# Kernel optimization log

Measured on AMD Instinct MI355X. Metric: run time of the kernel, lower is better.

## Reference

```python
import jax, jax.numpy as jnp
import numpy as np

B, N, C, H, K = 16, 2048, 64, 128, 16
EPS = 1e-5  # torch BatchNorm1d default eps


def _bn(h, g, b, axes):
    # training-mode batch norm: biased variance over all non-channel axes
    m = h.mean(axes, keepdims=True)
    v = h.var(axes, keepdims=True)
    return (h - m) * jax.lax.rsqrt(v + EPS) * g + b


def _edge_conv(x, W1, b1, g1, be1, W2, b2, g2, be2):
    # x: [B, N, C]; dynamic kNN graph in feature space (per graph), includes self
    sq = jnp.sum(x * x, axis=-1)                                   # [B, N]
    d2 = sq[:, :, None] + sq[:, None, :] - 2.0 * jnp.einsum('bnc,bmc->bnm', x, x)
    idx = jax.lax.top_k(-d2, K)[1]                                 # [B, N, K]
    xj = jax.vmap(lambda xb, ib: xb[ib])(x, idx)                   # [B, N, K, C]
    xi = jnp.broadcast_to(x[:, :, None, :], xj.shape)
    h = jnp.concatenate([xi, xj - xi], axis=-1) @ W1 + b1          # [B, N, K, H]
    h = jax.nn.relu(_bn(h, g1, be1, (0, 1, 2)))
    h = h @ W2 + b2
    h = jax.nn.relu(_bn(h, g2, be2, (0, 1, 2)))
    return h.max(axis=2)                                           # max aggregation -> [B, N, H]


def setup_inputs() -> dict:
    key = jax.random.key(0)
    ks = jax.random.split(key, 8)
    inp = {
        'x': jax.random.normal(ks[0], (B * N, C), jnp.float32),
        'batch': jnp.repeat(jnp.arange(B, dtype=jnp.int32), N),
    }
    i = 1
    for pref in ('s', 't'):
        inp[f'{pref}_W1'] = jax.random.normal(ks[i], (2 * C, H), jnp.float32) * 0.05; i += 1
        inp[f'{pref}_b1'] = jnp.zeros((H,), jnp.float32)
        inp[f'{pref}_g1'] = jnp.ones((H,), jnp.float32)
        inp[f'{pref}_be1'] = jnp.zeros((H,), jnp.float32)
        inp[f'{pref}_W2'] = jax.random.normal(ks[i], (H, H), jnp.float32) * 0.05; i += 1
        inp[f'{pref}_b2'] = jnp.zeros((H,), jnp.float32)
        inp[f'{pref}_g2'] = jnp.ones((H,), jnp.float32)
        inp[f'{pref}_be2'] = jnp.zeros((H,), jnp.float32)
    inp['f_W'] = jax.random.normal(ks[i], (2 * H, H), jnp.float32) * 0.05
    inp['f_b'] = jnp.zeros((H,), jnp.float32)
    inp['f_g'] = jnp.ones((H,), jnp.float32)
    inp['f_be'] = jnp.zeros((H,), jnp.float32)
    return inp


def reference(x, batch,
              s_W1, s_b1, s_g1, s_be1, s_W2, s_b2, s_g2, s_be2,
              t_W1, t_b1, t_g1, t_be1, t_W2, t_b2, t_g2, t_be2,
              f_W, f_b, f_g, f_be):
    # batch is sorted with B equal-size graphs of N nodes -> reshape
    xb = x.reshape(B, N, C)
    xs = _edge_conv(xb, s_W1, s_b1, s_g1, s_be1, s_W2, s_b2, s_g2, s_be2)
    xt = _edge_conv(xb, t_W1, t_b1, t_g1, t_be1, t_W2, t_b2, t_g2, t_be2)
    comb = jnp.concatenate([xs, xt], axis=-1).reshape(B * N, 2 * H)
    h = comb @ f_W + f_b
    return jax.nn.relu(_bn(h, f_g, f_be, (0,)))
```

## Files before the change

kernel.cpp:

```cpp
#include <hip/hip_runtime.h>
#include <hip/hip_bf16.h>
#include <stdint.h>

#define NB 16
#define NN 2048
#define NC 64
#define NH 128
#define NK 16
#define NS (NB*NN)
#define NSK (NS*NK)
#define EPSV 1e-5f

typedef __attribute__((ext_vector_type(8))) short short8;
typedef __attribute__((ext_vector_type(8))) _Float16 half8;
typedef __attribute__((ext_vector_type(8))) unsigned short ushort8;
typedef __attribute__((ext_vector_type(4))) float f32x4;

__device__ __forceinline__ unsigned short f2bf(float x) {
  union { float f; unsigned u; } v; v.f = x;
  unsigned r = v.u + 0x7fffu + ((v.u >> 16) & 1u);
  return (unsigned short)(r >> 16);
}

__device__ __forceinline__ unsigned orderf(float f) {
  unsigned u = __float_as_uint(f);
  return u ^ ((unsigned)((int)u >> 31) | 0x80000000u);
}

__device__ __forceinline__ float unorderf(unsigned whi) {
  return (whi == 0xffffffffu) ? __builtin_inff()
       : __uint_as_float((whi & 0x80000000u) ? (whi ^ 0x80000000u) : ~whi);
}

__device__ __forceinline__ unsigned long long shfl_xor_u64(unsigned long long v, int m) {
  unsigned lo = (unsigned)(v & 0xffffffffull);
  unsigned hi = (unsigned)(v >> 32);
  lo = __shfl_xor(lo, m, 64);
  hi = __shfl_xor(hi, m, 64);
  return (((unsigned long long)hi) << 32) | lo;
}

__global__ void prep_x(const float* __restrict__ x, float* __restrict__ sq,
                       unsigned short* __restrict__ xh, unsigned short* __restrict__ xl) {
  int i = blockIdx.x * blockDim.x + threadIdx.x;
  if (i >= NS) return;
  const float4* x4 = (const float4*)(x + (size_t)i * NC);
  float s = 0.f;
#pragma unroll
  for (int k = 0; k < 8; k++) {
    float4 a = x4[2*k], b = x4[2*k+1];
    float f[8] = {a.x,a.y,a.z,a.w,b.x,b.y,b.z,b.w};
    ushort8 hv, lv;
#pragma unroll
    for (int j = 0; j < 8; j++) {
      float v = f[j];
      s += v*v;
      _Float16 h = (_Float16)v;
      float r = v - (float)h;
      _Float16 l = (_Float16)r;
      union { _Float16 ff; unsigned short u; } ch, cl;
      ch.ff = h; cl.ff = l;
      hv[j] = ch.u; lv[j] = cl.u;
    }
    *(ushort8*)(xh + (size_t)i*64 + k*8) = hv;
    *(ushort8*)(xl + (size_t)i*64 + k*8) = lv;
  }
  sq[i] = s;
}

__global__ __launch_bounds__(256) void knn5_kernel(const unsigned short* __restrict__ xh,
                                                   const unsigned short* __restrict__ xl,
                                                   const float* __restrict__ sq,
                                                   int* __restrict__ nbr) {
  __shared__ unsigned short rAh[64*64], rAl[64*64];
  __shared__ unsigned short cBh[64*64], cBl[64*64];
  __shared__ float sqc[64];
  __shared__ float d2s[256*17];
  int b = blockIdx.x >> 5;
  int rb = blockIdx.x & 31;
  int w = threadIdx.x >> 6, lane = threadIdx.x & 63;
  int n16 = lane & 15, q = lane >> 4;
  int rowbase = b*NN + rb*64;
  float* myd2 = &d2s[threadIdx.x * 17];

  {
    int r = threadIdx.x >> 2;
    int c0 = (threadIdx.x & 3) * 2;
#pragma unroll
    for (int cc = 0; cc < 2; cc++) {
      int c = c0 + cc;
      int pos = (c ^ (r & 7)) * 8;
      *(ushort8*)&rAh[r*64 + pos] = *(const ushort8*)(xh + (size_t)(rowbase + r)*64 + c*8);
      *(ushort8*)&rAl[r*64 + pos] = *(const ushort8*)(xl + (size_t)(rowbase + r)*64 + c*8);
    }
  }
  __syncthreads();
  half8 bh[2], bl[2];
  int m = w*16 + n16;
#pragma unroll
  for (int ks = 0; ks < 2; ks++) {
    int pos = ((ks*4 + q) ^ (m & 7)) * 8;
    bh[ks] = *(const half8*)&rAh[m*64 + pos];
    bl[ks] = *(const half8*)&rAl[m*64 + pos];
  }
  float sqr = sq[rowbase + m];

  unsigned long long keys[16];
#pragma unroll
  for (int i = 0; i < 16; i++) keys[i] = ~0ull;
  float wd2 = __builtin_inff();

  for (int ch = 0; ch < 32; ch++) {
    int colbase = b*NN + ch*64;
    __syncthreads();
    {
      int r = threadIdx.x >> 2;
      int c0 = (threadIdx.x & 3) * 2;
#pragma unroll
      for (int cc = 0; cc < 2; cc++) {
        int c = c0 + cc;
        int pos = (c ^ (r & 7)) * 8;
        *(ushort8*)&cBh[r*64 + pos] = *(const ushort8*)(xh + (size_t)(colbase + r)*64 + c*8);
        *(ushort8*)&cBl[r*64 + pos] = *(const ushort8*)(xl + (size_t)(colbase + r)*64 + c*8);
      }
      if (threadIdx.x < 64) sqc[threadIdx.x] = sq[colbase + threadIdx.x];
    }
    __syncthreads();
    f32x4 acc[4];
#pragma unroll
    for (int ci = 0; ci < 4; ci++) acc[ci] = (f32x4){0.f,0.f,0.f,0.f};
#pragma unroll
    for (int ks = 0; ks < 2; ks++) {
#pragma unroll
      for (int ci = 0; ci < 4; ci++) {
        int n = ci*16 + n16;
        int pos = ((ks*4 + q) ^ (n & 7)) * 8;
        half8 ah_ = *(const half8*)&cBh[n*64 + pos];
        half8 al_ = *(const half8*)&cBl[n*64 + pos];
        acc[ci] = __builtin_amdgcn_mfma_f32_16x16x32_f16(ah_, bh[ks], acc[ci], 0, 0, 0);
        acc[ci] = __builtin_amdgcn_mfma_f32_16x16x32_f16(al_, bh[ks], acc[ci], 0, 0, 0);
        acc[ci] = __builtin_amdgcn_mfma_f32_16x16x32_f16(ah_, bl[ks], acc[ci], 0, 0, 0);
      }
    }
    float d2v[16];
    unsigned mask = 0;
#pragma unroll
    for (int ci = 0; ci < 4; ci++)
#pragma unroll
      for (int r = 0; r < 4; r++) {
        int idx = ci*4 + r;
        float d2 = fmaf(-2.f, acc[ci][r], sqr + sqc[ci*16 + q*4 + r]);
        d2v[idx] = d2;
        mask |= (d2 <= wd2) ? (1u << idx) : 0u;
      }
    if (mask) {
#pragma unroll
      for (int i = 0; i < 16; i++) myd2[i] = d2v[i];
      while (mask) {
        int i = __builtin_ctz(mask);
        mask &= mask - 1;
        float dd = myd2[i];
        if (dd > wd2) continue;
        int col = colbase + (i >> 2)*16 + q*4 + (i & 3);
        unsigned long long key = ((unsigned long long)orderf(dd) << 32) | (unsigned)col;
#pragma unroll
        for (int j = 0; j < 16; j++) {
          bool cl = key < keys[j];
          unsigned long long lo = cl ? key : keys[j];
          key = cl ? keys[j] : key;
          keys[j] = lo;
        }
        wd2 = fminf(wd2, unorderf((unsigned)(keys[15] >> 32)));
      }
    }
    {
      unsigned whi = (unsigned)(keys[15] >> 32);
      unsigned o = __shfl_xor(whi, 16, 64); whi = (o < whi) ? o : whi;
      o = __shfl_xor(whi, 32, 64); whi = (o < whi) ? o : whi;
      wd2 = unorderf(whi);
    }
  }
  for (int j = 0; j < NK; j++) {
    unsigned long long mk = keys[0];
#pragma unroll
    for (int i = 1; i < 16; i++) mk = (keys[i] < mk) ? keys[i] : mk;
    unsigned long long o = shfl_xor_u64(mk, 16); mk = (o < mk) ? o : mk;
    o = shfl_xor_u64(mk, 32); mk = (o < mk) ? o : mk;
#pragma unroll
    for (int i = 0; i < 16; i++) if (keys[i] == mk) keys[i] = ~0ull;
    if (q == 0) nbr[(size_t)(rowbase + m)*NK + j] = (int)(mk & 0xffffffffu);
  }
}

__global__ void prep_weights(const float* __restrict__ sW1, const float* __restrict__ sW2,
                             const float* __restrict__ tW1, const float* __restrict__ tW2,
                             const float* __restrict__ fW,
                             unsigned short* __restrict__ sW1t, unsigned short* __restrict__ sW2t,
                             unsigned short* __restrict__ tW1t, unsigned short* __restrict__ tW2t,
                             unsigned short* __restrict__ fWt) {
  int i = blockIdx.x * blockDim.x + threadIdx.x;
  if (i < 4*16384) {
    int mi = i >> 14, e = i & 16383;
    int h = e >> 7, k = e & 127;
    const float* src = (mi==0) ? sW1 : (mi==1) ? sW2 : (mi==2) ? tW1 : tW2;
    unsigned short* dst = (mi==0) ? sW1t : (mi==1) ? sW2t : (mi==2) ? tW1t : tW2t;
    dst[h*128 + k] = f2bf(src[k*128 + h]);
  } else {
    int e = i - 4*16384;
    if (e < 128*256) {
      int h = e >> 8, k = e & 255;
      fWt[h*256 + k] = f2bf(fW[k*128 + h]);
    }
  }
}

__global__ __launch_bounds__(256) void pnode_kernel(
    const float* __restrict__ x,
    const unsigned short* __restrict__ sW1t, const unsigned short* __restrict__ tW1t,
    float* __restrict__ PS, float* __restrict__ PT) {
  __shared__ unsigned short xt_[64*64];
  int rowbase = blockIdx.x * 64;
  int lane = threadIdx.x & 63;
  int wave = threadIdx.x >> 6;
  int n16 = lane & 15, q = lane >> 4;
  int cb = wave * 32;
  {
    int r = threadIdx.x >> 2, part = threadIdx.x & 3;
    const float4* xp = (const float4*)(x + (size_t)(rowbase + r) * NC) + part*4;
#pragma unroll
    for (int cc = 0; cc < 2; cc++) {
      int c = part*2 + cc;
      float4 a = xp[cc*2], b = xp[cc*2+1];
      int pos = (c ^ (r & 7)) * 8;
      unsigned short* d = &xt_[r*64 + pos];
      d[0]=f2bf(a.x); d[1]=f2bf(a.y); d[2]=f2bf(a.z); d[3]=f2bf(a.w);
      d[4]=f2bf(b.x); d[5]=f2bf(b.y); d[6]=f2bf(b.z); d[7]=f2bf(b.w);
    }
  }
  __syncthreads();
  f32x4 aS[4][2], aT[4][2];
#pragma unroll
  for (int ri = 0; ri < 4; ri++)
#pragma unroll
    for (int ci = 0; ci < 2; ci++) {
      aS[ri][ci] = (f32x4){0.f,0.f,0.f,0.f};
      aT[ri][ci] = (f32x4){0.f,0.f,0.f,0.f};
    }
#pragma unroll
  for (int ks = 0; ks < 2; ks++) {
    short8 af[4];
#pragma unroll
    for (int ri = 0; ri < 4; ri++) {
      int m = ri*16 + n16;
      af[ri] = *(const short8*)&xt_[m*64 + (((ks*4+q) ^ (m & 7)))*8];
    }
#pragma unroll
    for (int ci = 0; ci < 2; ci++) {
      int col = cb + ci*16 + n16;
      short8 bS = *(const short8*)(sW1t + col*128 + (ks*4+q)*8);
      short8 bT = *(const short8*)(tW1t + col*128 + (ks*4+q)*8);
#pragma unroll
      for (int ri = 0; ri < 4; ri++) {
        aS[ri][ci] = __builtin_amdgcn_mfma_f32_16x16x32_bf16(af[ri], bS, aS[ri][ci], 0, 0, 0);
        aT[ri][ci] = __builtin_amdgcn_mfma_f32_16x16x32_bf16(af[ri], bT, aT[ri][ci], 0, 0, 0);
      }
    }
  }
#pragma unroll
  for (int ri = 0; ri < 4; ri++)
#pragma unroll
    for (int ci = 0; ci < 2; ci++) {
      int col = cb + ci*16 + n16;
#pragma unroll
      for (int r = 0; r < 4; r++) {
        int row = rowbase + ri*16 + q*4 + r;
        PS[(size_t)row*128 + col] = aS[ri][ci][r];
        PT[(size_t)row*128 + col] = aT[ri][ci][r];
      }
    }
}

__global__ __launch_bounds__(256, 2) void dstat_kernel(
    const float* __restrict__ x, const int* __restrict__ nbr,
    const unsigned short* __restrict__ sW1t, const unsigned short* __restrict__ tW1t,
    const float* __restrict__ PS, const float* __restrict__ PT,
    unsigned short* __restrict__ D,
    float* __restrict__ statS, float* __restrict__ statT) {
  __shared__ unsigned short dlds[64*64];
  int wave = threadIdx.x >> 6, lane = threadIdx.x & 63;
  int n16 = lane & 15, q = lane >> 4;
  int cb = wave * 32;
  int g = blockIdx.x & 15, sub = blockIdx.x >> 4;
  float psS[2]={0,0}, ps2S[2]={0,0}, psT[2]={0,0}, ps2T[2]={0,0};

  for (int it = 0; it < 4; it++) {
    int tile = g*512 + sub*4 + it;
    __syncthreads();
    {
      int r4 = threadIdx.x >> 2, part = threadIdx.x & 3;
      int s = tile*64 + r4;
      int node = s >> 4;
      int ng = nbr[s];
      const float4* xi = (const float4*)(x + (size_t)node * NC) + part*4;
      const float4* xj = (const float4*)(x + (size_t)ng  * NC) + part*4;
      unsigned short* dstg = D + (size_t)tile*4096 + (size_t)r4*64;
#pragma unroll
      for (int cc = 0; cc < 2; cc++) {
        int c = part*2 + cc;
        float4 a0 = xi[cc*2], a1 = xi[cc*2+1];
        float4 b0 = xj[cc*2], b1 = xj[cc*2+1];
        int pos = (c ^ (r4 & 7)) * 8;
        ushort8 dv;
        dv[0]=f2bf(b0.x-a0.x); dv[1]=f2bf(b0.y-a0.y); dv[2]=f2bf(b0.z-a0.z); dv[3]=f2bf(b0.w-a0.w);
        dv[4]=f2bf(b1.x-a1.x); dv[5]=f2bf(b1.y-a1.y); dv[6]=f2bf(b1.z-a1.z); dv[7]=f2bf(b1.w-a1.w);
        *(ushort8*)(dstg + pos) = dv;
        *(ushort8*)(dlds + r4*64 + pos) = dv;
      }
    }
    __syncthreads();
    int node0 = tile*4;
    float pS[4][2], pT[4][2];
#pragma unroll
    for (int ri = 0; ri < 4; ri++)
#pragma unroll
      for (int ci = 0; ci < 2; ci++) {
        int col = cb + ci*16 + n16;
        pS[ri][ci] = PS[(size_t)(node0+ri)*128 + col];
        pT[ri][ci] = PT[(size_t)(node0+ri)*128 + col];
      }
    f32x4 aS[4][2], aT[4][2];
#pragma unroll
    for (int ri = 0; ri < 4; ri++)
#pragma unroll
      for (int ci = 0; ci < 2; ci++) {
        aS[ri][ci] = (f32x4){0.f,0.f,0.f,0.f};
        aT[ri][ci] = (f32x4){0.f,0.f,0.f,0.f};
      }
#pragma unroll
    for (int ks = 0; ks < 2; ks++) {
      short8 af[4];
#pragma unroll
      for (int ri = 0; ri < 4; ri++) {
        int m = ri*16 + n16;
        af[ri] = *(const short8*)&dlds[m*64 + ((ks*4+q) ^ (m & 7))*8];
      }
#pragma unroll
      for (int ci = 0; ci < 2; ci++) {
        int col = cb + ci*16 + n16;
        short8 bS = *(const short8*)(sW1t + col*128 + 64 + (ks*4+q)*8);
        short8 bT = *(const short8*)(tW1t + col*128 + 64 + (ks*4+q)*8);
#pragma unroll
        for (int ri = 0; ri < 4; ri++) {
          aS[ri][ci] = __builtin_amdgcn_mfma_f32_16x16x32_bf16(af[ri], bS, aS[ri][ci], 0, 0, 0);
          aT[ri][ci] = __builtin_amdgcn_mfma_f32_16x16x32_bf16(af[ri], bT, aT[ri][ci], 0, 0, 0);
        }
      }
    }
#pragma unroll
    for (int ci = 0; ci < 2; ci++)
#pragma unroll
      for (int ri = 0; ri < 4; ri++)
#pragma unroll
        for (int r = 0; r < 4; r++) {
          float vS = aS[ri][ci][r] + pS[ri][ci];
          float vT = aT[ri][ci][r] + pT[ri][ci];
          psS[ci] += vS; ps2S[ci] += vS*vS;
          psT[ci] += vT; ps2T[ci] += vT*vT;
        }
  }
#pragma unroll
  for (int ci = 0; ci < 2; ci++) {
    int col = cb + ci*16 + n16;
    float a = psS[ci], a2 = ps2S[ci], b2v = psT[ci], b3 = ps2T[ci];
    a   += __shfl_xor(a, 16, 64);   a   += __shfl_xor(a, 32, 64);
    a2  += __shfl_xor(a2, 16, 64);  a2  += __shfl_xor(a2, 32, 64);
    b2v += __shfl_xor(b2v, 16, 64); b2v += __shfl_xor(b2v, 32, 64);
    b3  += __shfl_xor(b3, 16, 64);  b3  += __shfl_xor(b3, 32, 64);
    if (q == 0) {
      atomicAdd(&statS[col], a);
      atomicAdd(&statS[128 + col], a2);
      atomicAdd(&statT[col], b2v);
      atomicAdd(&statT[128 + col], b3);
    }
  }
}

template<int MODE>
__global__ __launch_bounds__(256, 2) void mlp_pass2(
    const unsigned short* __restrict__ D,
    const float* __restrict__ PS, const float* __restrict__ PT,
    const unsigned short* __restrict__ sW1t, const unsigned short* __restrict__ sW2t,
    const unsigned short* __restrict__ tW1t, const unsigned short* __restrict__ tW2t,
    const unsigned short* __restrict__ fWt,
    const float* __restrict__ affS1, const float* __restrict__ affS2,
    const float* __restrict__ affT1, const float* __restrict__ affT2,
    float* __restrict__ statS, float* __restrict__ statT,
    float* __restrict__ statF, float* __restrict__ gout) {
  __shared__ unsigned short dlds[64*64];
  __shared__ unsigned short atile[64*128];
  __shared__ unsigned short xtile[(MODE == 2) ? 16*256 : 64];
  int wave = threadIdx.x >> 6;
  int lane = threadIdx.x & 63;
  int n16 = lane & 15, q = lane >> 4;
  int cb = wave * 32;

  float s1S[2], h1S[2], s2S[2], h2S[2];
  float s1T[2], h1T[2], s2T[2], h2T[2];
#pragma unroll
  for (int ci = 0; ci < 2; ci++) {
    int col = cb + ci*16 + n16;
    s1S[ci] = affS1[col]; h1S[ci] = affS1[128 + col];
    s1T[ci] = affT1[col]; h1T[ci] = affT1[128 + col];
  }
  if (MODE == 2) {
#pragma unroll
    for (int ci = 0; ci < 2; ci++) {
      int col = cb + ci*16 + n16;
      s2S[ci] = affS2[col]; h2S[ci] = affS2[128 + col];
      s2T[ci] = affT2[col]; h2T[ci] = affT2[128 + col];
    }
  }
  float psS[2] = {0,0}, ps2S[2] = {0,0};
  float psT[2] = {0,0}, ps2T[2] = {0,0};

  for (int it = 0; it < 4; it++) {
    int tile = blockIdx.x*4 + it;
    __syncthreads();
    {
      const ushort8* src = (const ushort8*)(D + (size_t)tile*4096);
      ushort8* dst = (ushort8*)dlds;
      dst[threadIdx.x] = src[threadIdx.x];
      dst[threadIdx.x + 256] = src[threadIdx.x + 256];
    }
    __syncthreads();
    int node0 = tile*4;
    float pS[4][2], pT[4][2];
#pragma unroll
    for (int ri = 0; ri < 4; ri++)
#pragma unroll
      for (int ci = 0; ci < 2; ci++) {
        int col = cb + ci*16 + n16;
        pS[ri][ci] = PS[(size_t)(node0+ri)*128 + col];
        pT[ri][ci] = PT[(size_t)(node0+ri)*128 + col];
      }

#pragma unroll
    for (int st = 0; st < 2; st++) {
      const unsigned short* W1t = st ? tW1t : sW1t;
      const unsigned short* W2t = st ? tW2t : sW2t;
      const float* sc1 = st ? s1T : s1S;  const float* sh1 = st ? h1T : h1S;
      const float* sc2 = st ? s2T : s2S;  const float* sh2 = st ? h2T : h2S;
      float (*pp)[2] = st ? pT : pS;
      float* ps  = st ? psT : psS;
      float* ps2 = st ? ps2T : ps2S;

      f32x4 acc[4][2];
#pragma unroll
      for (int ri = 0; ri < 4; ri++)
#pragma unroll
        for (int ci = 0; ci < 2; ci++)
          acc[ri][ci] = (f32x4){0.f,0.f,0.f,0.f};
#pragma unroll
      for (int ks = 0; ks < 2; ks++) {
        short8 af[4], bf[2];
#pragma unroll
        for (int ri = 0; ri < 4; ri++) {
          int mm = ri*16 + n16;
          af[ri] = *(const short8*)&dlds[mm*64 + ((ks*4+q) ^ (mm & 7))*8];
        }
#pragma unroll
        for (int ci = 0; ci < 2; ci++) {
          int col = cb + ci*16 + n16;
          bf[ci] = *(const short8*)(W1t + col*128 + 64 + (ks*4+q)*8);
        }
#pragma unroll
        for (int ri = 0; ri < 4; ri++)
#pragma unroll
          for (int ci = 0; ci < 2; ci++)
            acc[ri][ci] = __builtin_amdgcn_mfma_f32_16x16x32_bf16(af[ri], bf[ci], acc[ri][ci], 0, 0, 0);
      }
#pragma unroll
      for (int ri = 0; ri < 4; ri++)
#pragma unroll
        for (int ci = 0; ci < 2; ci++) {
          int colL = cb + ci*16 + n16;
          int kc8 = colL >> 3;
#pragma unroll
          for (int r = 0; r < 4; r++) {
            float v = acc[ri][ci][r] + pp[ri][ci];
            v = fmaxf(v * sc1[ci] + sh1[ci], 0.f);
            int rowL = ri*16 + q*4 + r;
            int pos = ((kc8 ^ (rowL & 7)) << 3) + (colL & 7);
            atile[rowL*128 + pos] = f2bf(v);
          }
        }
      __syncthreads();
      f32x4 acc2[4][2];
#pragma unroll
      for (int ri = 0; ri < 4; ri++)
#pragma unroll
        for (int ci = 0; ci < 2; ci++)
          acc2[ri][ci] = (f32x4){0.f,0.f,0.f,0.f};
#pragma unroll
      for (int ks = 0; ks < 4; ks++) {
        short8 a2[4], bf[2];
#pragma unroll
        for (int ri = 0; ri < 4; ri++) {
          int mm = ri*16 + n16;
          int kc8 = (ks*4 + q) ^ (mm & 7);
          a2[ri] = *(const short8*)&atile[mm*128 + kc8*8];
        }
#pragma unroll
        for (int ci = 0; ci < 2; ci++) {
          int col = cb + ci*16 + n16;
          bf[ci] = *(const short8*)(W2t + col*128 + ks*32 + q*8);
        }
#pragma unroll
        for (int ri = 0; ri < 4; ri++)
#pragma unroll
          for (int ci = 0; ci < 2; ci++)
            acc2[ri][ci] = __builtin_amdgcn_mfma_f32_16x16x32_bf16(a2[ri], bf[ci], acc2[ri][ci], 0, 0, 0);
      }
      if (MODE == 1) {
#pragma unroll
        for (int ci = 0; ci < 2; ci++)
#pragma unroll
          for (int ri = 0; ri < 4; ri++)
#pragma unroll
            for (int r = 0; r < 4; r++) {
              float v = acc2[ri][ci][r];
              ps[ci] += v; ps2[ci] += v*v;
            }
      } else {
#pragma unroll
        for (int ri = 0; ri < 4; ri++)
#pragma unroll
          for (int ci = 0; ci < 2; ci++) {
            int col = cb + ci*16 + n16;
            float vm = 0.f;
#pragma unroll
            for (int r = 0; r < 4; r++) {
              float v = fmaxf(acc2[ri][ci][r] * sc2[ci] + sh2[ci], 0.f);
              vm = fmaxf(vm, v);
            }
            vm = fmaxf(vm, __shfl_xor(vm, 16, 64));
            vm = fmaxf(vm, __shfl_xor(vm, 32, 64));
            if (q == 0) {
              int ln = it*4 + ri;
              int fcol = st*128 + col;
              int kc8 = fcol >> 3;
              int pos = ((kc8 ^ (ln & 7)) << 3) + (fcol & 7);
              xtile[ln*256 + pos] = f2bf(vm);
            }
          }
      }
      if (st == 0) __syncthreads();
    }
  }
  if (MODE == 1) {
#pragma unroll
    for (int ci = 0; ci < 2; ci++) {
      int col = cb + ci*16 + n16;
      float a = psS[ci], a2 = ps2S[ci], b = psT[ci], b2 = ps2T[ci];
      a  += __shfl_xor(a, 16, 64);  a  += __shfl_xor(a, 32, 64);
      a2 += __shfl_xor(a2, 16, 64); a2 += __shfl_xor(a2, 32, 64);
      b  += __shfl_xor(b, 16, 64);  b  += __shfl_xor(b, 32, 64);
      b2 += __shfl_xor(b2, 16, 64); b2 += __shfl_xor(b2, 32, 64);
      if (q == 0) {
        atomicAdd(&statS[col], a);
        atomicAdd(&statS[128 + col], a2);
        atomicAdd(&statT[col], b);
        atomicAdd(&statT[128 + col], b2);
      }
    }
  } else {
    __syncthreads();
    f32x4 facc[2];
#pragma unroll
    for (int ci = 0; ci < 2; ci++) facc[ci] = (f32x4){0.f,0.f,0.f,0.f};
#pragma unroll
    for (int ks = 0; ks < 8; ks++) {
      int kc8 = (ks*4 + q) ^ (n16 & 7);
      short8 af = *(const short8*)&xtile[n16*256 + kc8*8];
#pragma unroll
      for (int ci = 0; ci < 2; ci++) {
        int col = cb + ci*16 + n16;
        short8 bf = *(const short8*)(fWt + col*256 + ks*32 + q*8);
        facc[ci] = __builtin_amdgcn_mfma_f32_16x16x32_bf16(af, bf, facc[ci], 0, 0, 0);
      }
    }
    int nodeBase = blockIdx.x * 16;
    float fs[2] = {0,0}, fs2[2] = {0,0};
#pragma unroll
    for (int ci = 0; ci < 2; ci++) {
      int col = cb + ci*16 + n16;
#pragma unroll
      for (int r = 0; r < 4; r++) {
        float v = facc[ci][r];
        gout[(size_t)(nodeBase + q*4 + r)*128 + col] = v;
        fs[ci] += v; fs2[ci] += v*v;
      }
      float a = fs[ci], a2 = fs2[ci];
      a  += __shfl_xor(a, 16, 64);  a  += __shfl_xor(a, 32, 64);
      a2 += __shfl_xor(a2, 16, 64); a2 += __shfl_xor(a2, 32, 64);
      if (q == 0) {
        atomicAdd(&statF[col], a);
        atomicAdd(&statF[128 + col], a2);
      }
    }
  }
}

__global__ void finalize_kernel(const float* __restrict__ stats,
                                const float* __restrict__ g,
                                const float* __restrict__ be,
                                float* __restrict__ aff, float invcount) {
  int c = threadIdx.x;
  if (c < 128) {
    float mean = stats[c] * invcount;
    float var = stats[128 + c] * invcount - mean*mean;
    float scale = g[c] / sqrtf(var + EPSV);
    aff[c] = scale;
    aff[128 + c] = be[c] - mean * scale;
  }
}

__global__ void apply_bn_kernel(float* __restrict__ out, const float* __restrict__ aff) {
  int i = blockIdx.x * blockDim.x + threadIdx.x;
  if (i < NS*NH) {
    int c = i & 127;
    out[i] = fmaxf(out[i] * aff[c] + aff[128 + c], 0.f);
  }
}

extern "C" void kernel_launch(void* const* d_in, const int* in_sizes, int n_in,
                              void* d_out, int out_size, void* d_ws, size_t ws_size,
                              hipStream_t stream) {
  const float* x   = (const float*)d_in[0];
  const float* sW1 = (const float*)d_in[2];
  const float* sg1 = (const float*)d_in[4];
  const float* sbe1= (const float*)d_in[5];
  const float* sW2 = (const float*)d_in[6];
  const float* sg2 = (const float*)d_in[8];
  const float* sbe2= (const float*)d_in[9];
  const float* tW1 = (const float*)d_in[10];
  const float* tg1 = (const float*)d_in[12];
  const float* tbe1= (const float*)d_in[13];
  const float* tW2 = (const float*)d_in[14];
  const float* tg2 = (const float*)d_in[16];
  const float* tbe2= (const float*)d_in[17];
  const float* fW  = (const float*)d_in[18];
  const float* fg  = (const float*)d_in[20];
  const float* fbe = (const float*)d_in[21];
  float* out = (float*)d_out;

  char* w = (char*)d_ws;
  float* sq = (float*)w;                 w += (size_t)NS*4;
  int* nbr = (int*)w;                    w += (size_t)NSK*4;
  unsigned short* sW1t = (unsigned short*)w; w += 32768;
  unsigned short* sW2t = (unsigned short*)w; w += 32768;
  unsigned short* tW1t = (unsigned short*)w; w += 32768;
  unsigned short* tW2t = (unsigned short*)w; w += 32768;
  unsigned short* fWt  = (unsigned short*)w; w += 65536;
  float* stats = (float*)w;              w += 2560*4;
  unsigned short* xh = (unsigned short*)w; w += (size_t)NS*64*2;
  unsigned short* xl = (unsigned short*)w; w += (size_t)NS*64*2;
  unsigned short* Dg = (unsigned short*)w; w += (size_t)NSK*64*2;
  float* PS = (float*)w;                 w += (size_t)NS*128*4;
  float* PT = (float*)w;                 w += (size_t)NS*128*4;

  float* st_s1 = stats;        float* af_s1 = stats + 256;
  float* st_s2 = stats + 512;  float* af_s2 = stats + 768;
  float* st_t1 = stats + 1024; float* af_t1 = stats + 1280;
  float* st_t2 = stats + 1536; float* af_t2 = stats + 1792;
  float* st_f  = stats + 2048; float* af_f  = stats + 2304;

  hipMemsetAsync(stats, 0, 2560*4, stream);
  prep_weights<<<(4*16384 + 128*256 + 255)/256, 256, 0, stream>>>(
      sW1, sW2, tW1, tW2, fW, sW1t, sW2t, tW1t, tW2t, fWt);
  prep_x<<<NS/256, 256, 0, stream>>>(x, sq, xh, xl);
  knn5_kernel<<<NB*32, 256, 0, stream>>>(xh, xl, sq, nbr);
  pnode_kernel<<<NS/64, 256, 0, stream>>>(x, sW1t, tW1t, PS, PT);
  dstat_kernel<<<2048, 256, 0, stream>>>(x, nbr, sW1t, tW1t, PS, PT, Dg, st_s1, st_t1);

  const float inv1 = 1.f/(float)NSK, invf = 1.f/(float)NS;
  finalize_kernel<<<1,128,0,stream>>>(st_s1, sg1, sbe1, af_s1, inv1);
  finalize_kernel<<<1,128,0,stream>>>(st_t1, tg1, tbe1, af_t1, inv1);
  mlp_pass2<1><<<2048,256,0,stream>>>(Dg, PS, PT, sW1t, sW2t, tW1t, tW2t, fWt,
      af_s1, nullptr, af_t1, nullptr, st_s2, st_t2, nullptr, nullptr);
  finalize_kernel<<<1,128,0,stream>>>(st_s2, sg2, sbe2, af_s2, inv1);
  finalize_kernel<<<1,128,0,stream>>>(st_t2, tg2, tbe2, af_t2, inv1);
  mlp_pass2<2><<<2048,256,0,stream>>>(Dg, PS, PT, sW1t, sW2t, tW1t, tW2t, fWt,
      af_s1, af_s2, af_t1, af_t2, nullptr, nullptr, st_f, out);
  finalize_kernel<<<1,128,0,stream>>>(st_f, fg, fbe, af_f, invf);
  apply_bn_kernel<<<(NS*NH)/256, 256, 0, stream>>>(out, af_f);
}
```

Measured before the change: 564.5 us.

## Store per-node max/min of second-layer preactivations to skip recomputing MLP

The first MLP pass now records, per node and channel, the max and min of the pre-BN second-layer outputs over the K neighbors, alongside the BN statistics. Because BN plus ReLU is monotone per channel (increasing or decreasing depending on the sign of the scale), the aggregated max can be recovered from the stored max or min. This lets the second full recomputation of both edge MLPs be replaced by a light kernel that applies the affine and ReLU and runs the final linear layer. The cost is writing and reading four NS x 128 fp32 buffers.

```diff
diff --git a/kernel.cpp b/kernel.cpp
--- a/kernel.cpp
+++ b/kernel.cpp
@@ -385,40 +385,28 @@
   }
 }
 
-template<int MODE>
-__global__ __launch_bounds__(256, 2) void mlp_pass2(
+__global__ __launch_bounds__(256, 2) void mlp_mid(
     const unsigned short* __restrict__ D,
     const float* __restrict__ PS, const float* __restrict__ PT,
     const unsigned short* __restrict__ sW1t, const unsigned short* __restrict__ sW2t,
     const unsigned short* __restrict__ tW1t, const unsigned short* __restrict__ tW2t,
-    const unsigned short* __restrict__ fWt,
-    const float* __restrict__ affS1, const float* __restrict__ affS2,
-    const float* __restrict__ affT1, const float* __restrict__ affT2,
+    const float* __restrict__ affS1, const float* __restrict__ affT1,
     float* __restrict__ statS, float* __restrict__ statT,
-    float* __restrict__ statF, float* __restrict__ gout) {
+    float* __restrict__ HmxS, float* __restrict__ HmnS,
+    float* __restrict__ HmxT, float* __restrict__ HmnT) {
   __shared__ unsigned short dlds[64*64];
   __shared__ unsigned short atile[64*128];
-  __shared__ unsigned short xtile[(MODE == 2) ? 16*256 : 64];
   int wave = threadIdx.x >> 6;
   int lane = threadIdx.x & 63;
   int n16 = lane & 15, q = lane >> 4;
   int cb = wave * 32;
 
-  float s1S[2], h1S[2], s2S[2], h2S[2];
-  float s1T[2], h1T[2], s2T[2], h2T[2];
+  float s1S[2], h1S[2], s1T[2], h1T[2];
 #pragma unroll
   for (int ci = 0; ci < 2; ci++) {
     int col = cb + ci*16 + n16;
     s1S[ci] = affS1[col]; h1S[ci] = affS1[128 + col];
     s1T[ci] = affT1[col]; h1T[ci] = affT1[128 + col];
-  }
-  if (MODE == 2) {
-#pragma unroll
-    for (int ci = 0; ci < 2; ci++) {
-      int col = cb + ci*16 + n16;
-      s2S[ci] = affS2[col]; h2S[ci] = affS2[128 + col];
-      s2T[ci] = affT2[col]; h2T[ci] = affT2[128 + col];
-    }
   }
   float psS[2] = {0,0}, ps2S[2] = {0,0};
   float psT[2] = {0,0}, ps2T[2] = {0,0};
@@ -449,10 +437,11 @@
       const unsigned short* W1t = st ? tW1t : sW1t;
       const unsigned short* W2t = st ? tW2t : sW2t;
       const float* sc1 = st ? s1T : s1S;  const float* sh1 = st ? h1T : h1S;
-      const float* sc2 = st ? s2T : s2S;  const float* sh2 = st ? h2T : h2S;
       float (*pp)[2] = st ? pT : pS;
       float* ps  = st ? psT : psS;
       float* ps2 = st ? ps2T : ps2S;
+      float* Hmx = st ? HmxT : HmxS;
+      float* Hmn = st ? HmnT : HmnS;
 
       f32x4 acc[4][2];
 #pragma unroll
@@ -521,92 +510,143 @@
           for (int ci = 0; ci < 2; ci++)
             acc2[ri][ci] = __builtin_amdgcn_mfma_f32_16x16x32_bf16(a2[ri], bf[ci], acc2[ri][ci], 0, 0, 0);
       }
-      if (MODE == 1) {
-#pragma unroll
-        for (int ci = 0; ci < 2; ci++)
-#pragma unroll
-          for (int ri = 0; ri < 4; ri++)
-#pragma unroll
-            for (int r = 0; r < 4; r++) {
-              float v = acc2[ri][ci][r];
-              ps[ci] += v; ps2[ci] += v*v;
-            }
-      } else {
-#pragma unroll
-        for (int ri = 0; ri < 4; ri++)
-#pragma unroll
-          for (int ci = 0; ci < 2; ci++) {
-            int col = cb + ci*16 + n16;
-            float vm = 0.f;
-#pragma unroll
-            for (int r = 0; r < 4; r++) {
-              float v = fmaxf(acc2[ri][ci][r] * sc2[ci] + sh2[ci], 0.f);
-              vm = fmaxf(vm, v);
-            }
-            vm = fmaxf(vm, __shfl_xor(vm, 16, 64));
-            vm = fmaxf(vm, __shfl_xor(vm, 32, 64));
-            if (q == 0) {
-              int ln = it*4 + ri;
-              int fcol = st*128 + col;
-              int kc8 = fcol >> 3;
-              int pos = ((kc8 ^ (ln & 7)) << 3) + (fcol & 7);
-              xtile[ln*256 + pos] = f2bf(vm);
-            }
+#pragma unroll
+      for (int ri = 0; ri < 4; ri++)
+#pragma unroll
+        for (int ci = 0; ci < 2; ci++) {
+          int col = cb + ci*16 + n16;
+          float vmx = -__builtin_inff(), vmn = __builtin_inff();
+#pragma unroll
+          for (int r = 0; r < 4; r++) {
+            float v = acc2[ri][ci][r];
+            ps[ci] += v; ps2[ci] += v*v;
+            vmx = fmaxf(vmx, v); vmn = fminf(vmn, v);
           }
-      }
+          vmx = fmaxf(vmx, __shfl_xor(vmx, 16, 64));
+          vmx = fmaxf(vmx, __shfl_xor(vmx, 32, 64));
+          vmn = fminf(vmn, __shfl_xor(vmn, 16, 64));
+          vmn = fminf(vmn, __shfl_xor(vmn, 32, 64));
+          if (q == 0) {
+            Hmx[(size_t)(node0 + ri)*128 + col] = vmx;
+            Hmn[(size_t)(node0 + ri)*128 + col] = vmn;
+          }
+        }
       if (st == 0) __syncthreads();
     }
   }
-  if (MODE == 1) {
+#pragma unroll
+  for (int ci = 0; ci < 2; ci++) {
+    int col = cb + ci*16 + n16;
+    float a = psS[ci], a2 = ps2S[ci], b = psT[ci], b2 = ps2T[ci];
+    a  += __shfl_xor(a, 16, 64);  a  += __shfl_xor(a, 32, 64);
+    a2 += __shfl_xor(a2, 16, 64); a2 += __shfl_xor(a2, 32, 64);
+    b  += __shfl_xor(b, 16, 64);  b  += __shfl_xor(b, 32, 64);
+    b2 += __shfl_xor(b2, 16, 64); b2 += __shfl_xor(b2, 32, 64);
+    if (q == 0) {
+      atomicAdd(&statS[col], a);
+      atomicAdd(&statS[128 + col], a2);
+      atomicAdd(&statT[col], b);
+      atomicAdd(&statT[128 + col], b2);
+    }
+  }
+}
+
+__global__ __launch_bounds__(256) void final2_kernel(
+    const float* __restrict__ HmxS, const float* __restrict__ HmnS,
+    const float* __restrict__ HmxT, const float* __restrict__ HmnT,
+    const float* __restrict__ affS2, const float* __restrict__ affT2,
+    const unsigned short* __restrict__ fWt,
+    float* __restrict__ gout, float* __restrict__ statF) {
+  __shared__ unsigned short xtile[64*256];
+  __shared__ float aff[512];
+  int tid = threadIdx.x;
+  aff[tid] = affS2[tid & 255];
+  aff[256 + tid] = affT2[tid & 255];
+  __syncthreads();
+  int node0 = blockIdx.x * 64;
+  {
+    int r = tid >> 2, part = tid & 3;
+    size_t rowoff = (size_t)(node0 + r) * 128;
+#pragma unroll
+    for (int st = 0; st < 2; st++) {
+      const float* Hmx = st ? HmxT : HmxS;
+      const float* Hmn = st ? HmnT : HmnS;
+      const float* af = &aff[st*256];
+#pragma unroll
+      for (int g8 = 0; g8 < 4; g8++) {
+        int col0 = part*32 + g8*8;
+        float4 x0 = *(const float4*)&Hmx[rowoff + col0];
+        float4 x1 = *(const float4*)&Hmx[rowoff + col0 + 4];
+        float4 n0 = *(const float4*)&Hmn[rowoff + col0];
+        float4 n1 = *(const float4*)&Hmn[rowoff + col0 + 4];
+        float mx[8] = {x0.x,x0.y,x0.z,x0.w,x1.x,x1.y,x1.z,x1.w};
+        float mn[8] = {n0.x,n0.y,n0.z,n0.w,n1.x,n1.y,n1.z,n1.w};
+        ushort8 ov;
+#pragma unroll
+        for (int j = 0; j < 8; j++) {
+          int col = col0 + j;
+          float sc = af[col], sh = af[128 + col];
+          float z = (sc >= 0.f) ? mx[j] : mn[j];
+          ov[j] = f2bf(fmaxf(sc*z + sh, 0.f));
+        }
+        int kc8 = (st*128 + col0) >> 3;
+        *(ushort8*)&xtile[r*256 + ((kc8 ^ (r & 7)) << 3)] = ov;
+      }
+    }
+  }
+  __syncthreads();
+  int wave = tid >> 6, lane = tid & 63;
+  int n16 = lane & 15, q = lane >> 4;
+  int cb = wave * 32;
+  f32x4 acc[4][2];
+#pragma unroll
+  for (int ri = 0; ri < 4; ri++)
+#pragma unroll
+    for (int ci = 0; ci < 2; ci++)
+      acc[ri][ci] = (f32x4){0.f,0.f,0.f,0.f};
+#pragma unroll
+  for (int ks = 0; ks < 8; ks++) {
+    short8 af[4], bf[2];
+#pragma unroll
+    for (int ri = 0; ri < 4; ri++) {
+      int mm = ri*16 + n16;
+      int kc8 = (ks*4 + q) ^ (mm & 7);
+      af[ri] = *(const short8*)&xtile[mm*256 + kc8*8];
+    }
 #pragma unroll
     for (int ci = 0; ci < 2; ci++) {
       int col = cb + ci*16 + n16;
-      float a = psS[ci], a2 = ps2S[ci], b = psT[ci], b2 = ps2T[ci];
-      a  += __shfl_xor(a, 16, 64);  a  += __shfl_xor(a, 32, 64);
-      a2 += __shfl_xor(a2, 16, 64); a2 += __shfl_xor(a2, 32, 64);
-      b  += __shfl_xor(b, 16, 64);  b  += __shfl_xor(b, 32, 64);
-      b2 += __shfl_xor(b2, 16, 64); b2 += __shfl_xor(b2, 32, 64);
-      if (q == 0) {
-        atomicAdd(&statS[col], a);
-        atomicAdd(&statS[128 + col], a2);
-        atomicAdd(&statT[col], b);
-        atomicAdd(&statT[128 + col], b2);
-      }
-    }
-  } else {
-    __syncthreads();
-    f32x4 facc[2];
-#pragma unroll
-    for (int ci = 0; ci < 2; ci++) facc[ci] = (f32x4){0.f,0.f,0.f,0.f};
-#pragma unroll
-    for (int ks = 0; ks < 8; ks++) {
-      int kc8 = (ks*4 + q) ^ (n16 & 7);
-      short8 af = *(const short8*)&xtile[n16*256 + kc8*8];
-#pragma unroll
-      for (int ci = 0; ci < 2; ci++) {
-        int col = cb + ci*16 + n16;
-        short8 bf = *(const short8*)(fWt + col*256 + ks*32 + q*8);
-        facc[ci] = __builtin_amdgcn_mfma_f32_16x16x32_bf16(af, bf, facc[ci], 0, 0, 0);
-      }
-    }
-    int nodeBase = blockIdx.x * 16;
-    float fs[2] = {0,0}, fs2[2] = {0,0};
+      bf[ci] = *(const short8*)(fWt + col*256 + ks*32 + q*8);
+    }
+#pragma unroll
+    for (int ri = 0; ri < 4; ri++)
+#pragma unroll
+      for (int ci = 0; ci < 2; ci++)
+        acc[ri][ci] = __builtin_amdgcn_mfma_f32_16x16x32_bf16(af[ri], bf[ci], acc[ri][ci], 0, 0, 0);
+  }
+  float ps[2] = {0,0}, ps2[2] = {0,0};
+#pragma unroll
+  for (int ri = 0; ri < 4; ri++)
 #pragma unroll
     for (int ci = 0; ci < 2; ci++) {
       int col = cb + ci*16 + n16;
 #pragma unroll
       for (int r = 0; r < 4; r++) {
-        float v = facc[ci][r];
-        gout[(size_t)(nodeBase + q*4 + r)*128 + col] = v;
-        fs[ci] += v; fs2[ci] += v*v;
-      }
-      float a = fs[ci], a2 = fs2[ci];
-      a  += __shfl_xor(a, 16, 64);  a  += __shfl_xor(a, 32, 64);
-      a2 += __shfl_xor(a2, 16, 64); a2 += __shfl_xor(a2, 32, 64);
-      if (q == 0) {
-        atomicAdd(&statF[col], a);
-        atomicAdd(&statF[128 + col], a2);
-      }
+        float v = acc[ri][ci][r];
+        int row = node0 + ri*16 + q*4 + r;
+        gout[(size_t)row*128 + col] = v;
+        ps[ci] += v; ps2[ci] += v*v;
+      }
+    }
+#pragma unroll
+  for (int ci = 0; ci < 2; ci++) {
+    int col = cb + ci*16 + n16;
+    float a = ps[ci], a2 = ps2[ci];
+    a  += __shfl_xor(a, 16, 64);  a  += __shfl_xor(a, 32, 64);
+    a2 += __shfl_xor(a2, 16, 64); a2 += __shfl_xor(a2, 32, 64);
+    if (q == 0) {
+      atomicAdd(&statF[col], a);
+      atomicAdd(&statF[128 + col], a2);
     }
   }
 }
@@ -668,6 +708,10 @@
   unsigned short* Dg = (unsigned short*)w; w += (size_t)NSK*64*2;
   float* PS = (float*)w;                 w += (size_t)NS*128*4;
   float* PT = (float*)w;                 w += (size_t)NS*128*4;
+  float* HmxS = (float*)w;               w += (size_t)NS*128*4;
+  float* HmnS = (float*)w;               w += (size_t)NS*128*4;
+  float* HmxT = (float*)w;               w += (size_t)NS*128*4;
+  float* HmnT = (float*)w;               w += (size_t)NS*128*4;
 
   float* st_s1 = stats;        float* af_s1 = stats + 256;
   float* st_s2 = stats + 512;  float* af_s2 = stats + 768;
@@ -686,12 +730,12 @@
   const float inv1 = 1.f/(float)NSK, invf = 1.f/(float)NS;
   finalize_kernel<<<1,128,0,stream>>>(st_s1, sg1, sbe1, af_s1, inv1);
   finalize_kernel<<<1,128,0,stream>>>(st_t1, tg1, tbe1, af_t1, inv1);
-  mlp_pass2<1><<<2048,256,0,stream>>>(Dg, PS, PT, sW1t, sW2t, tW1t, tW2t, fWt,
-      af_s1, nullptr, af_t1, nullptr, st_s2, st_t2, nullptr, nullptr);
+  mlp_mid<<<2048,256,0,stream>>>(Dg, PS, PT, sW1t, sW2t, tW1t, tW2t,
+      af_s1, af_t1, st_s2, st_t2, HmxS, HmnS, HmxT, HmnT);
   finalize_kernel<<<1,128,0,stream>>>(st_s2, sg2, sbe2, af_s2, inv1);
   finalize_kernel<<<1,128,0,stream>>>(st_t2, tg2, tbe2, af_t2, inv1);
-  mlp_pass2<2><<<2048,256,0,stream>>>(Dg, PS, PT, sW1t, sW2t, tW1t, tW2t, fWt,
-      af_s1, af_s2, af_t1, af_t2, nullptr, nullptr, st_f, out);
+  final2_kernel<<<NS/64, 256, 0, stream>>>(HmxS, HmnS, HmxT, HmnT,
+      af_s2, af_t2, fWt, out, st_f);
   finalize_kernel<<<1,128,0,stream>>>(st_f, fg, fbe, af_f, invf);
   apply_bn_kernel<<<(NS*NH)/256, 256, 0, stream>>>(out, af_f);
 }
```

New measurement: 505.9 us. -10.4%, faster.
